# Kernel optimization log

Measured on AMD Instinct MI355X. Metric: run time of the kernel, lower is better.

## Reference

```python
import jax, jax.numpy as jnp
import numpy as np

BN_EPS = 1e-5
LN_EPS = 1e-5

N_NODES = 50000
N_EDGES = 800000
D_IN = 128
D_HID = 512


def _batchnorm(h, gamma, beta):
    # training-mode BatchNorm1d: biased variance over the node/batch dim
    m = jnp.mean(h, axis=0)
    v = jnp.mean(jnp.square(h - m), axis=0)
    return (h - m) * jax.lax.rsqrt(v + BN_EPS) * gamma + beta


def setup_inputs() -> dict:
    key = jax.random.key(0)
    ks = jax.random.split(key, 8)
    x = jax.random.normal(ks[0], (N_NODES, D_IN), dtype=jnp.float32)
    edge_index = jax.random.randint(ks[1], (2, N_EDGES), 0, N_NODES, dtype=jnp.int64)
    s1 = 1.0 / np.sqrt(D_IN)
    s2 = 1.0 / np.sqrt(D_HID)
    W1 = jax.random.uniform(ks[2], (D_IN, D_HID), jnp.float32, -s1, s1)
    b1 = jax.random.uniform(ks[3], (D_HID,), jnp.float32, -s1, s1)
    W2 = jax.random.uniform(ks[4], (D_HID, D_IN), jnp.float32, -s2, s2)
    b2 = jax.random.uniform(ks[5], (D_IN,), jnp.float32, -s2, s2)
    return {
        "x": x,
        "edge_index": edge_index,
        "W1": W1, "b1": b1,
        "bn1_g": jnp.ones((D_HID,), jnp.float32), "bn1_b": jnp.zeros((D_HID,), jnp.float32),
        "W2": W2, "b2": b2,
        "bn2_g": jnp.ones((D_IN,), jnp.float32), "bn2_b": jnp.zeros((D_IN,), jnp.float32),
        "ln_g": jnp.ones((D_IN,), jnp.float32), "ln_b": jnp.zeros((D_IN,), jnp.float32),
    }


def reference(x, edge_index, W1, b1, bn1_g, bn1_b, W2, b2, bn2_g, bn2_b, ln_g, ln_b):
    n = x.shape[0]
    src = edge_index[0]
    dst = edge_index[1]
    # GIN aggregation: sum of neighbor (source) features at each destination node
    agg = jax.ops.segment_sum(x[src], dst, num_segments=n)  # [N, D_IN]
    h = x + agg  # (1 + eps) * x + agg, eps = 0
    # MLP: Linear -> BN -> ReLU -> Linear -> BN -> ReLU (final activation)
    h = jax.nn.relu(_batchnorm(h @ W1 + b1, bn1_g, bn1_b))  # [N, D_HID]
    h = jax.nn.relu(_batchnorm(h @ W2 + b2, bn2_g, bn2_b))  # [N, D_IN]
    # residual + LayerNorm (dropout p=0 -> identity)
    out = h + x
    m = jnp.mean(out, axis=-1, keepdims=True)
    v = jnp.mean(jnp.square(out - m), axis=-1, keepdims=True)
    out = (out - m) * jax.lax.rsqrt(v + LN_EPS) * ln_g + ln_b
    return out
```

## Files before the change

### kernel.cpp

```cpp
#include <hip/hip_runtime.h>
#include <stdint.h>

#define N_NODES 50000
#define N_EDGES 800000
#define D_IN    128
#define D_HID   512
#define NPAD    50048
#define SCAN_NB 196

typedef __attribute__((ext_vector_type(8))) short short8;
typedef __attribute__((ext_vector_type(4))) float f32x4;

union Pack8 { unsigned short us[8]; uint4 v; };

__device__ __forceinline__ float bf2f(unsigned short u) {
    union { unsigned int i; float f; } v; v.i = ((unsigned int)u) << 16; return v.f;
}
__device__ __forceinline__ unsigned short f2bf(float f) {
    union { float f; unsigned int i; } v; v.f = f;
    unsigned int r = v.i + 0x7fffu + ((v.i >> 16) & 1u);
    return (unsigned short)(r >> 16);
}
__device__ __forceinline__ float loadP(const void* p, long i, int isf) {
    return isf ? ((const float*)p)[i] : bf2f(((const unsigned short*)p)[i]);
}
__device__ __forceinline__ uint4 pack8(float4 f0, float4 f1) {
    Pack8 p;
    p.us[0] = f2bf(f0.x); p.us[1] = f2bf(f0.y); p.us[2] = f2bf(f0.z); p.us[3] = f2bf(f0.w);
    p.us[4] = f2bf(f1.x); p.us[5] = f2bf(f1.y); p.us[6] = f2bf(f1.z); p.us[7] = f2bf(f1.w);
    return p.v;
}

__global__ void k_init(const void* __restrict__ x, const int* __restrict__ ei,
                       float* __restrict__ stats, int* __restrict__ counts,
                       int* __restrict__ flags) {
    int t = threadIdx.x;
    if (blockIdx.x < 201) {
        int i = blockIdx.x * 256 + t;
        if (i < 1280) stats[i] = 0.f;
        else if (i < 1280 + N_NODES) counts[i - 1280] = 0;
    } else {
        __shared__ int sh[2];
        if (t == 0) { sh[0] = 0; sh[1] = 1; }
        __syncthreads();
        const unsigned short* xu = (const unsigned short*)x;
        for (int i = t; i < 8192; i += 256)
            if (((xu[i] >> 7) & 0xFF) == 0xFF) sh[0] = 1;
        for (int k = t; k < 64; k += 256)
            if (ei[2 * k + 1] != 0) sh[1] = 0;
        __syncthreads();
        if (t == 0) { flags[0] = sh[0]; flags[1] = sh[1]; }
    }
}

__global__ void k_transpose2(const void* __restrict__ W1, const void* __restrict__ W2,
                             unsigned short* __restrict__ w1t, unsigned short* __restrict__ w2t,
                             const int* __restrict__ flags) {
    int isf = flags[0];
    int idx = blockIdx.x * 256 + threadIdx.x;
    if (idx < D_IN * D_HID) {
        int k = idx / D_HID, n = idx % D_HID;
        w1t[n * D_IN + k] = isf ? f2bf(((const float*)W1)[idx])
                                : ((const unsigned short*)W1)[idx];
    } else {
        int j = idx - D_IN * D_HID;
        int k = j / D_IN, n = j % D_IN;
        w2t[n * D_HID + k] = isf ? f2bf(((const float*)W2)[j])
                                 : ((const unsigned short*)W2)[j];
    }
}

__global__ void k_count(const int* __restrict__ ei, int* __restrict__ counts,
                        const int* __restrict__ flags) {
    int i64 = flags[1];
    int e = blockIdx.x * 256 + threadIdx.x;
    int d = i64 ? ei[2 * N_EDGES + 2 * e] : ei[N_EDGES + e];
    d = min(max(d, 0), N_NODES - 1);
    atomicAdd(&counts[d], 1);
}

__global__ __launch_bounds__(256) void k_scan_block(const int* __restrict__ counts,
                                                    int* __restrict__ rowptr,
                                                    int* __restrict__ partials) {
    __shared__ int a[256], b[256];
    int t = threadIdx.x;
    int idx = blockIdx.x * 256 + t;
    int c = (idx < N_NODES) ? counts[idx] : 0;
    a[t] = c;
    __syncthreads();
    int* src = a; int* dst = b;
    for (int off = 1; off < 256; off <<= 1) {
        dst[t] = src[t] + ((t >= off) ? src[t - off] : 0);
        __syncthreads();
        int* tmp = src; src = dst; dst = tmp;
    }
    if (idx < N_NODES) rowptr[idx] = src[t] - c;
    if (t == 255) partials[blockIdx.x] = src[255];
}

__global__ __launch_bounds__(256) void k_scan_part(int* __restrict__ partials) {
    __shared__ int a[256], b[256];
    int t = threadIdx.x;
    int c = (t < SCAN_NB) ? partials[t] : 0;
    a[t] = c;
    __syncthreads();
    int* src = a; int* dst = b;
    for (int off = 1; off < 256; off <<= 1) {
        dst[t] = src[t] + ((t >= off) ? src[t - off] : 0);
        __syncthreads();
        int* tmp = src; src = dst; dst = tmp;
    }
    if (t < SCAN_NB) partials[t] = src[t] - c;
}

__global__ void k_scan_add(int* __restrict__ rowptr, int* __restrict__ cursor,
                           const int* __restrict__ partials) {
    int idx = blockIdx.x * 256 + threadIdx.x;
    if (idx < N_NODES) {
        int v = rowptr[idx] + partials[blockIdx.x];
        rowptr[idx] = v;
        cursor[idx] = v;
    } else if (idx == N_NODES) {
        rowptr[N_NODES] = N_EDGES;
    }
}

__global__ void k_fill(const int* __restrict__ ei, int* __restrict__ cursor,
                       int* __restrict__ bucket, const int* __restrict__ flags) {
    int i64 = flags[1];
    int e = blockIdx.x * 256 + threadIdx.x;
    int s, d;
    if (i64) { s = ei[2 * e]; d = ei[2 * N_EDGES + 2 * e]; }
    else     { s = ei[e];     d = ei[N_EDGES + e]; }
    s = min(max(s, 0), N_NODES - 1);
    d = min(max(d, 0), N_NODES - 1);
    int pos = atomicAdd(&cursor[d], 1);
    bucket[pos] = s;
}

__global__ __launch_bounds__(256) void k_gather(const int* __restrict__ rowptr,
                                                const int* __restrict__ bucket,
                                                const void* __restrict__ x,
                                                float* __restrict__ agg,
                                                const int* __restrict__ flags) {
    int isf = flags[0];
    int w = threadIdx.x >> 6, lane = threadIdx.x & 63;
    int row = blockIdx.x * 4 + w;
    float a0 = 0.f, a1 = 0.f;
    if (row < N_NODES) {
        int beg = rowptr[row], end = rowptr[row + 1];
        if (isf) {
            const float* xf = (const float*)x;
            float2 v = *(const float2*)(xf + (size_t)row * D_IN + lane * 2);
            a0 = v.x; a1 = v.y;
            int j = beg;
            for (; j + 4 <= end; j += 4) {
                int s0 = bucket[j], s1 = bucket[j + 1], s2 = bucket[j + 2], s3 = bucket[j + 3];
                float2 n0 = *(const float2*)(xf + (size_t)s0 * D_IN + lane * 2);
                float2 n1 = *(const float2*)(xf + (size_t)s1 * D_IN + lane * 2);
                float2 n2 = *(const float2*)(xf + (size_t)s2 * D_IN + lane * 2);
                float2 n3 = *(const float2*)(xf + (size_t)s3 * D_IN + lane * 2);
                a0 += (n0.x + n1.x) + (n2.x + n3.x);
                a1 += (n0.y + n1.y) + (n2.y + n3.y);
            }
            for (; j < end; j++) {
                float2 n = *(const float2*)(xf + (size_t)bucket[j] * D_IN + lane * 2);
                a0 += n.x; a1 += n.y;
            }
        } else {
            const unsigned int* xu = (const unsigned int*)x;
            unsigned int u = xu[(size_t)row * 64 + lane];
            a0 = bf2f(u & 0xffff); a1 = bf2f(u >> 16);
            int j = beg;
            for (; j + 4 <= end; j += 4) {
                int s0 = bucket[j], s1 = bucket[j + 1], s2 = bucket[j + 2], s3 = bucket[j + 3];
                unsigned int u0 = xu[(size_t)s0 * 64 + lane];
                unsigned int u1 = xu[(size_t)s1 * 64 + lane];
                unsigned int u2 = xu[(size_t)s2 * 64 + lane];
                unsigned int u3 = xu[(size_t)s3 * 64 + lane];
                a0 += (bf2f(u0 & 0xffff) + bf2f(u1 & 0xffff)) + (bf2f(u2 & 0xffff) + bf2f(u3 & 0xffff));
                a1 += (bf2f(u0 >> 16) + bf2f(u1 >> 16)) + (bf2f(u2 >> 16) + bf2f(u3 >> 16));
            }
            for (; j < end; j++) {
                unsigned int n = xu[(size_t)bucket[j] * 64 + lane];
                a0 += bf2f(n & 0xffff); a1 += bf2f(n >> 16);
            }
        }
    }
    *(float2*)(agg + (size_t)row * D_IN + lane * 2) = make_float2(a0, a1);
}

__global__ __launch_bounds__(256) void k_g1stats(const float* __restrict__ agg,
                                                 const unsigned short* __restrict__ w1t,
                                                 const void* __restrict__ b1,
                                                 float* __restrict__ sum1,
                                                 float* __restrict__ sumsq1,
                                                 const int* __restrict__ flags) {
    __shared__ unsigned short ldsX[128 * 128];
    __shared__ unsigned short ldsW[128 * 128];
    int isf = flags[0];
    int t = threadIdx.x;
    int m0 = blockIdx.x * 128;
    int r = t >> 1, half = t & 1;
#pragma unroll
    for (int i = 0; i < 8; i++) {
        int chunk = half * 8 + i;
        int sw = ((chunk ^ (r & 15)) * 8);
        const float* g = agg + (size_t)(m0 + r) * D_IN + chunk * 8;
        *(uint4*)(ldsX + r * 128 + sw) = pack8(*(const float4*)g, *(const float4*)(g + 4));
    }
    int wid = t >> 6, lane = t & 63;
    int wm = wid & 1, wn = wid >> 1;
    int quad = lane >> 4, l16 = lane & 15;
    for (int nb = 0; nb < 4; nb++) {
        __syncthreads();
#pragma unroll
        for (int i = 0; i < 8; i++) {
            int chunk = half * 8 + i;
            *(uint4*)(ldsW + r * 128 + ((chunk ^ (r & 15)) * 8)) =
                *(const uint4*)(w1t + (size_t)(nb * 128 + r) * D_IN + chunk * 8);
        }
        __syncthreads();
        f32x4 acc[4][4] = {};
#pragma unroll
        for (int ks = 0; ks < 4; ks++) {
            short8 af[4], bfr[4];
#pragma unroll
            for (int mt = 0; mt < 4; mt++)
                af[mt] = *(const short8*)(ldsX + (wm * 64 + mt * 16 + l16) * 128 + (((ks * 4 + quad) ^ l16) * 8));
#pragma unroll
            for (int nt = 0; nt < 4; nt++)
                bfr[nt] = *(const short8*)(ldsW + (wn * 64 + nt * 16 + l16) * 128 + (((ks * 4 + quad) ^ l16) * 8));
#pragma unroll
            for (int mt = 0; mt < 4; mt++)
#pragma unroll
                for (int nt = 0; nt < 4; nt++)
                    acc[mt][nt] = __builtin_amdgcn_mfma_f32_16x16x32_bf16(af[mt], bfr[nt], acc[mt][nt], 0, 0, 0);
        }
#pragma unroll
        for (int nt = 0; nt < 4; nt++) {
            int n = nb * 128 + wn * 64 + nt * 16 + l16;
            float bias = loadP(b1, n, isf);
            float s = 0.f, ss = 0.f;
#pragma unroll
            for (int mt = 0; mt < 4; mt++) {
                int Rb = m0 + wm * 64 + mt * 16 + quad * 4;
#pragma unroll
                for (int rg = 0; rg < 4; rg++) {
                    if (Rb + rg < N_NODES) {
                        float z = acc[mt][nt][rg] + bias;
                        s += z; ss += z * z;
                    }
                }
            }
            s += __shfl_xor(s, 16, 64); ss += __shfl_xor(ss, 16, 64);
            s += __shfl_xor(s, 32, 64); ss += __shfl_xor(ss, 32, 64);
            if (quad == 0) { atomicAdd(&sum1[n], s); atomicAdd(&sumsq1[n], ss); }
        }
    }
}

__global__ __launch_bounds__(256) void k_fused(const float* __restrict__ agg,
                                               const unsigned short* __restrict__ w1t,
                                               const unsigned short* __restrict__ w2t,
                                               const void* __restrict__ b1,
                                               const void* __restrict__ b2,
                                               const void* __restrict__ g1,
                                               const void* __restrict__ bb1,
                                               const float* __restrict__ sum1,
                                               const float* __restrict__ sumsq1,
                                               float* __restrict__ h2,
                                               float* __restrict__ sum2,
                                               float* __restrict__ sumsq2,
                                               const int* __restrict__ flags) {
    __shared__ unsigned short bufXP[128 * 128];
    __shared__ unsigned short bufW[128 * 128];
    int isf = flags[0];
    int t = threadIdx.x;
    int m0 = blockIdx.x * 128;
    int r = t >> 1, half = t & 1;
    int wid = t >> 6, lane = t & 63;
    int wm = wid & 1, wn = wid >> 1;
    int quad = lane >> 4, l16 = lane & 15;
    f32x4 acc2[4][4] = {};
    for (int nb = 0; nb < 4; nb++) {
        __syncthreads();
#pragma unroll
        for (int i = 0; i < 8; i++) {
            int chunk = half * 8 + i;
            int sw = ((chunk ^ (r & 15)) * 8);
            const float* g = agg + (size_t)(m0 + r) * D_IN + chunk * 8;
            *(uint4*)(bufXP + r * 128 + sw) = pack8(*(const float4*)g, *(const float4*)(g + 4));
            *(uint4*)(bufW + r * 128 + sw) = *(const uint4*)(w1t + (size_t)(nb * 128 + r) * D_IN + chunk * 8);
        }
        __syncthreads();
        f32x4 acc1[4][4] = {};
#pragma unroll
        for (int ks = 0; ks < 4; ks++) {
            short8 af[4], bfr[4];
#pragma unroll
            for (int mt = 0; mt < 4; mt++)
                af[mt] = *(const short8*)(bufXP + (wm * 64 + mt * 16 + l16) * 128 + (((ks * 4 + quad) ^ l16) * 8));
#pragma unroll
            for (int nt = 0; nt < 4; nt++)
                bfr[nt] = *(const short8*)(bufW + (wn * 64 + nt * 16 + l16) * 128 + (((ks * 4 + quad) ^ l16) * 8));
#pragma unroll
            for (int mt = 0; mt < 4; mt++)
#pragma unroll
                for (int nt = 0; nt < 4; nt++)
                    acc1[mt][nt] = __builtin_amdgcn_mfma_f32_16x16x32_bf16(af[mt], bfr[nt], acc1[mt][nt], 0, 0, 0);
        }
        __syncthreads();
#pragma unroll
        for (int nt = 0; nt < 4; nt++) {
            int nl = wn * 64 + nt * 16 + l16;
            int n1 = nb * 128 + nl;
            float mz = sum1[n1] * (1.f / N_NODES);
            float vz = sumsq1[n1] * (1.f / N_NODES) - mz * mz;
            float inv = rsqrtf(fmaxf(vz, 0.f) + 1e-5f);
            float A = loadP(g1, n1, isf) * inv;
            float C = loadP(bb1, n1, isf) - mz * A + loadP(b1, n1, isf) * A;
            int ccw = nl >> 3, cl = nl & 7;
#pragma unroll
            for (int mt = 0; mt < 4; mt++)
#pragma unroll
                for (int rg = 0; rg < 4; rg++) {
                    int R = wm * 64 + mt * 16 + quad * 4 + rg;
                    float z = fmaxf(acc1[mt][nt][rg] * A + C, 0.f);
                    bufXP[R * 128 + ((ccw ^ (R & 15)) * 8) + cl] = f2bf(z);
                }
        }
#pragma unroll
        for (int i = 0; i < 8; i++) {
            int chunk = half * 8 + i;
            *(uint4*)(bufW + r * 128 + ((chunk ^ (r & 15)) * 8)) =
                *(const uint4*)(w2t + (size_t)r * D_HID + nb * 128 + chunk * 8);
        }
        __syncthreads();
#pragma unroll
        for (int ks = 0; ks < 4; ks++) {
            short8 af[4], bfr[4];
#pragma unroll
            for (int mt = 0; mt < 4; mt++)
                af[mt] = *(const short8*)(bufXP + (wm * 64 + mt * 16 + l16) * 128 + (((ks * 4 + quad) ^ l16) * 8));
#pragma unroll
            for (int nt = 0; nt < 4; nt++)
                bfr[nt] = *(const short8*)(bufW + (wn * 64 + nt * 16 + l16) * 128 + (((ks * 4 + quad) ^ l16) * 8));
#pragma unroll
            for (int mt = 0; mt < 4; mt++)
#pragma unroll
                for (int nt = 0; nt < 4; nt++)
                    acc2[mt][nt] = __builtin_amdgcn_mfma_f32_16x16x32_bf16(af[mt], bfr[nt], acc2[mt][nt], 0, 0, 0);
        }
    }
#pragma unroll
    for (int nt = 0; nt < 4; nt++) {
        int n = wn * 64 + nt * 16 + l16;
        float bias = loadP(b2, n, isf);
        float s = 0.f, ss = 0.f;
#pragma unroll
        for (int mt = 0; mt < 4; mt++) {
            int Rb = m0 + wm * 64 + mt * 16 + quad * 4;
#pragma unroll
            for (int rg = 0; rg < 4; rg++) {
                float z = acc2[mt][nt][rg] + bias;
                h2[(size_t)(Rb + rg) * D_IN + n] = z;
                if (Rb + rg < N_NODES) { s += z; ss += z * z; }
            }
        }
        s += __shfl_xor(s, 16, 64); ss += __shfl_xor(ss, 16, 64);
        s += __shfl_xor(s, 32, 64); ss += __shfl_xor(ss, 32, 64);
        if (quad == 0) { atomicAdd(&sum2[n], s); atomicAdd(&sumsq2[n], ss); }
    }
}

__global__ __launch_bounds__(256) void k_final(const float* __restrict__ h2,
                                               const void* __restrict__ x,
                                               const float* __restrict__ sum2,
                                               const float* __restrict__ sumsq2,
                                               const void* __restrict__ g2,
                                               const void* __restrict__ bb2,
                                               const void* __restrict__ lng,
                                               const void* __restrict__ lnb,
                                               void* __restrict__ out,
                                               const int* __restrict__ flags) {
    int isf = flags[0];
    __shared__ float a2s[D_IN], c2s[D_IN];
    int t = threadIdx.x;
    if (t < D_IN) {
        float m = sum2[t] * (1.f / N_NODES);
        float v = sumsq2[t] * (1.f / N_NODES) - m * m;
        float inv = rsqrtf(fmaxf(v, 0.f) + 1e-5f);
        float a = loadP(g2, t, isf) * inv;
        a2s[t] = a;
        c2s[t] = loadP(bb2, t, isf) - m * a;
    }
    __syncthreads();
    int w = t >> 6, lane = t & 63;
    int row = blockIdx.x * 4 + w;
    if (row >= N_NODES) return;
    size_t base = (size_t)row * D_IN;
    float o0 = fmaxf(a2s[lane] * h2[base + lane] + c2s[lane], 0.f) + loadP(x, base + lane, isf);
    float o1 = fmaxf(a2s[lane + 64] * h2[base + 64 + lane] + c2s[lane + 64], 0.f) + loadP(x, base + 64 + lane, isf);
    float s = o0 + o1, ss = o0 * o0 + o1 * o1;
#pragma unroll
    for (int m = 1; m < 64; m <<= 1) {
        s += __shfl_xor(s, m, 64);
        ss += __shfl_xor(ss, m, 64);
    }
    float mean = s * (1.f / D_IN);
    float var = ss * (1.f / D_IN) - mean * mean;
    float inv = rsqrtf(fmaxf(var, 0.f) + 1e-5f);
    float r0 = (o0 - mean) * inv * loadP(lng, lane, isf) + loadP(lnb, lane, isf);
    float r1 = (o1 - mean) * inv * loadP(lng, lane + 64, isf) + loadP(lnb, lane + 64, isf);
    if (isf) {
        ((float*)out)[base + lane] = r0;
        ((float*)out)[base + 64 + lane] = r1;
    } else {
        ((unsigned short*)out)[base + lane] = f2bf(r0);
        ((unsigned short*)out)[base + 64 + lane] = f2bf(r1);
    }
}

extern "C" void kernel_launch(void* const* d_in, const int* in_sizes, int n_in,
                              void* d_out, int out_size, void* d_ws, size_t ws_size,
                              hipStream_t stream) {
    const void* x    = d_in[0];
    const int*  ei   = (const int*)d_in[1];
    const void* W1   = d_in[2];
    const void* b1   = d_in[3];
    const void* bn1g = d_in[4];
    const void* bn1b = d_in[5];
    const void* W2   = d_in[6];
    const void* b2   = d_in[7];
    const void* bn2g = d_in[8];
    const void* bn2b = d_in[9];
    const void* lng  = d_in[10];
    const void* lnb  = d_in[11];

    char* ws = (char*)d_ws;
    float* stats    = (float*)ws;
    float* sum1     = stats;
    float* sumsq1   = stats + 512;
    float* sum2     = stats + 1024;
    float* sumsq2   = stats + 1152;
    int*   flags    = (int*)(ws + 5120);
    int*   partials = (int*)(ws + 5184);
    int*   rowptr   = (int*)(ws + 8192);
    int*   cursor   = (int*)(ws + 212992);
    unsigned short* w1t = (unsigned short*)(ws + 417792);
    unsigned short* w2t = (unsigned short*)(ws + 548864);
    int*   bucket = (int*)(ws + 679936);
    float* agg    = (float*)(ws + 3879936);
    float* h2     = agg;

    k_init<<<202, 256, 0, stream>>>(x, ei, stats, cursor, flags);
    k_transpose2<<<512, 256, 0, stream>>>(W1, W2, w1t, w2t, flags);
    k_count<<<N_EDGES / 256, 256, 0, stream>>>(ei, cursor, flags);
    k_scan_block<<<SCAN_NB, 256, 0, stream>>>(cursor, rowptr, partials);
    k_scan_part<<<1, 256, 0, stream>>>(partials);
    k_scan_add<<<SCAN_NB, 256, 0, stream>>>(rowptr, cursor, partials);
    k_fill<<<N_EDGES / 256, 256, 0, stream>>>(ei, cursor, bucket, flags);
    k_gather<<<NPAD / 4, 256, 0, stream>>>(rowptr, bucket, x, agg, flags);
    k_g1stats<<<NPAD / 128, 256, 0, stream>>>(agg, w1t, b1, sum1, sumsq1, flags);
    k_fused<<<NPAD / 128, 256, 0, stream>>>(agg, w1t, w2t, b1, b2, bn1g, bn1b,
                                            sum1, sumsq1, h2, sum2, sumsq2, flags);
    k_final<<<(N_NODES + 3) / 4, 256, 0, stream>>>(h2, x, sum2, sumsq2, bn2g, bn2b, lng, lnb, d_out, flags);
}
```

Before: 383.3 us.

## Materialize GEMM1 output in bf16 instead of recomputing it in fused kernel

Replaces the stats-only GEMM1 pass plus the recompute-GEMM1 fused kernel with two kernels. The first computes GEMM1 once, accumulates BN1 statistics and writes the hidden activations to a bf16 workspace buffer. The second applies BN1+ReLU while loading that buffer, then runs GEMM2 and accumulates BN2 statistics. This removes the duplicate GEMM1 compute but adds roughly 100MB of extra HBM write and read traffic, and it only runs when the workspace is large enough.

```diff
diff --git a/kernel.cpp b/kernel.cpp
--- a/kernel.cpp
+++ b/kernel.cpp
@@ -190,6 +190,194 @@
     *(float2*)(agg + (size_t)row * D_IN + lane * 2) = make_float2(a0, a1);
 }
 
+
+__global__ __launch_bounds__(256) void k_g1h1(const float* __restrict__ agg,
+                                              const unsigned short* __restrict__ w1t,
+                                              const void* __restrict__ b1,
+                                              float* __restrict__ sum1,
+                                              float* __restrict__ sumsq1,
+                                              unsigned short* __restrict__ h1,
+                                              const int* __restrict__ flags) {
+    __shared__ unsigned short ldsX[64 * 128];
+    __shared__ unsigned short ldsW[128 * 128];
+    int isf = flags[0];
+    int t = threadIdx.x;
+    int m0 = blockIdx.x * 64;
+    {
+        int r = t >> 2;
+        const float* g = agg + (size_t)(m0 + r) * D_IN;
+#pragma unroll
+        for (int i = 0; i < 4; i++) {
+            int chunk = (t & 3) * 4 + i;
+            *(uint4*)(ldsX + r * 128 + ((chunk ^ (r & 15)) * 8)) =
+                pack8(*(const float4*)(g + chunk * 8), *(const float4*)(g + chunk * 8 + 4));
+        }
+    }
+    int wid = t >> 6, lane = t & 63;
+    int wm = wid & 1, wn = wid >> 1;
+    int quad = lane >> 4, l16 = lane & 15;
+    int r2 = t >> 1, half = t & 1;
+    for (int nb = 0; nb < 4; nb++) {
+        __syncthreads();
+#pragma unroll
+        for (int i = 0; i < 8; i++) {
+            int chunk = half * 8 + i;
+            *(uint4*)(ldsW + r2 * 128 + ((chunk ^ (r2 & 15)) * 8)) =
+                *(const uint4*)(w1t + (size_t)(nb * 128 + r2) * D_IN + chunk * 8);
+        }
+        __syncthreads();
+        f32x4 acc[2][4] = {};
+#pragma unroll
+        for (int ks = 0; ks < 4; ks++) {
+            short8 af[2], bfr[4];
+#pragma unroll
+            for (int mt = 0; mt < 2; mt++) {
+                int rr = wm * 32 + mt * 16 + l16;
+                af[mt] = *(const short8*)(ldsX + rr * 128 + (((ks * 4 + quad) ^ (rr & 15)) * 8));
+            }
+#pragma unroll
+            for (int nt = 0; nt < 4; nt++) {
+                int nn = wn * 64 + nt * 16 + l16;
+                bfr[nt] = *(const short8*)(ldsW + nn * 128 + (((ks * 4 + quad) ^ (nn & 15)) * 8));
+            }
+#pragma unroll
+            for (int mt = 0; mt < 2; mt++)
+#pragma unroll
+                for (int nt = 0; nt < 4; nt++)
+                    acc[mt][nt] = __builtin_amdgcn_mfma_f32_16x16x32_bf16(af[mt], bfr[nt], acc[mt][nt], 0, 0, 0);
+        }
+        __syncthreads();
+#pragma unroll
+        for (int nt = 0; nt < 4; nt++) {
+            int nl = wn * 64 + nt * 16 + l16;
+            int n = nb * 128 + nl;
+            float bias = loadP(b1, n, isf);
+            float s = 0.f, ss = 0.f;
+            int ccw = nl >> 3, cl = nl & 7;
+#pragma unroll
+            for (int mt = 0; mt < 2; mt++) {
+                int Rl = wm * 32 + mt * 16 + quad * 4;
+#pragma unroll
+                for (int rg = 0; rg < 4; rg++) {
+                    float z = acc[mt][nt][rg] + bias;
+                    ldsW[(Rl + rg) * 128 + ((ccw ^ ((Rl + rg) & 15)) * 8) + cl] = f2bf(z);
+                    if (m0 + Rl + rg < N_NODES) { s += z; ss += z * z; }
+                }
+            }
+            s += __shfl_xor(s, 16, 64); ss += __shfl_xor(ss, 16, 64);
+            s += __shfl_xor(s, 32, 64); ss += __shfl_xor(ss, 32, 64);
+            if (quad == 0) { atomicAdd(&sum1[n], s); atomicAdd(&sumsq1[n], ss); }
+        }
+        __syncthreads();
+        {
+            int r = t >> 2;
+            unsigned short* gh = h1 + (size_t)(m0 + r) * D_HID + nb * 128;
+#pragma unroll
+            for (int i = 0; i < 4; i++) {
+                int chunk = (t & 3) * 4 + i;
+                *(uint4*)(gh + chunk * 8) = *(const uint4*)(ldsW + r * 128 + ((chunk ^ (r & 15)) * 8));
+            }
+        }
+    }
+}
+
+__global__ __launch_bounds__(256) void k_bn1gemm2(const unsigned short* __restrict__ h1,
+                                                  const unsigned short* __restrict__ w2t,
+                                                  const void* __restrict__ b2,
+                                                  const void* __restrict__ g1,
+                                                  const void* __restrict__ bb1,
+                                                  const float* __restrict__ sum1,
+                                                  const float* __restrict__ sumsq1,
+                                                  float* __restrict__ h2,
+                                                  float* __restrict__ sum2,
+                                                  float* __restrict__ sumsq2,
+                                                  const int* __restrict__ flags) {
+    __shared__ unsigned short ldsP[64 * 128];
+    __shared__ unsigned short ldsW[128 * 128];
+    __shared__ float a1s[D_HID], c1s[D_HID];
+    int isf = flags[0];
+    int t = threadIdx.x;
+    int m0 = blockIdx.x * 64;
+    for (int k = t; k < D_HID; k += 256) {
+        float mz = sum1[k] * (1.f / N_NODES);
+        float vz = sumsq1[k] * (1.f / N_NODES) - mz * mz;
+        float inv = rsqrtf(fmaxf(vz, 0.f) + 1e-5f);
+        float A = loadP(g1, k, isf) * inv;
+        a1s[k] = A;
+        c1s[k] = loadP(bb1, k, isf) - mz * A;
+    }
+    int wid = t >> 6, lane = t & 63;
+    int wm = wid & 1, wn = wid >> 1;
+    int quad = lane >> 4, l16 = lane & 15;
+    int r2 = t >> 1, half = t & 1;
+    f32x4 acc[2][4] = {};
+    for (int kb = 0; kb < 4; kb++) {
+        __syncthreads();
+        {
+            int r = t >> 2;
+            const unsigned short* gh = h1 + (size_t)(m0 + r) * D_HID + kb * 128;
+#pragma unroll
+            for (int i = 0; i < 4; i++) {
+                int chunk = (t & 3) * 4 + i;
+                Pack8 raw, outv;
+                raw.v = *(const uint4*)(gh + chunk * 8);
+#pragma unroll
+                for (int j = 0; j < 8; j++) {
+                    int k = kb * 128 + chunk * 8 + j;
+                    outv.us[j] = f2bf(fmaxf(bf2f(raw.us[j]) * a1s[k] + c1s[k], 0.f));
+                }
+                *(uint4*)(ldsP + r * 128 + ((chunk ^ (r & 15)) * 8)) = outv.v;
+            }
+        }
+#pragma unroll
+        for (int i = 0; i < 8; i++) {
+            int chunk = half * 8 + i;
+            *(uint4*)(ldsW + r2 * 128 + ((chunk ^ (r2 & 15)) * 8)) =
+                *(const uint4*)(w2t + (size_t)r2 * D_HID + kb * 128 + chunk * 8);
+        }
+        __syncthreads();
+#pragma unroll
+        for (int ks = 0; ks < 4; ks++) {
+            short8 af[2], bfr[4];
+#pragma unroll
+            for (int mt = 0; mt < 2; mt++) {
+                int rr = wm * 32 + mt * 16 + l16;
+                af[mt] = *(const short8*)(ldsP + rr * 128 + (((ks * 4 + quad) ^ (rr & 15)) * 8));
+            }
+#pragma unroll
+            for (int nt = 0; nt < 4; nt++) {
+                int nn = wn * 64 + nt * 16 + l16;
+                bfr[nt] = *(const short8*)(ldsW + nn * 128 + (((ks * 4 + quad) ^ (nn & 15)) * 8));
+            }
+#pragma unroll
+            for (int mt = 0; mt < 2; mt++)
+#pragma unroll
+                for (int nt = 0; nt < 4; nt++)
+                    acc[mt][nt] = __builtin_amdgcn_mfma_f32_16x16x32_bf16(af[mt], bfr[nt], acc[mt][nt], 0, 0, 0);
+        }
+    }
+#pragma unroll
+    for (int nt = 0; nt < 4; nt++) {
+        int n = wn * 64 + nt * 16 + l16;
+        float bias = loadP(b2, n, isf);
+        float s = 0.f, ss = 0.f;
+#pragma unroll
+        for (int mt = 0; mt < 2; mt++) {
+            int Rb = m0 + wm * 32 + mt * 16 + quad * 4;
+#pragma unroll
+            for (int rg = 0; rg < 4; rg++) {
+                float z = acc[mt][nt][rg] + bias;
+                h2[(size_t)(Rb + rg) * D_IN + n] = z;
+                if (Rb + rg < N_NODES) { s += z; ss += z * z; }
+            }
+        }
+        s += __shfl_xor(s, 16, 64); ss += __shfl_xor(ss, 16, 64);
+        s += __shfl_xor(s, 32, 64); ss += __shfl_xor(ss, 32, 64);
+        if (quad == 0) { atomicAdd(&sum2[n], s); atomicAdd(&sumsq2[n], ss); }
+    }
+}
+
+
 __global__ __launch_bounds__(256) void k_g1stats(const float* __restrict__ agg,
                                                  const unsigned short* __restrict__ w1t,
                                                  const void* __restrict__ b1,
@@ -453,6 +641,8 @@
     int*   bucket = (int*)(ws + 679936);
     float* agg    = (float*)(ws + 3879936);
     float* h2     = agg;
+    unsigned short* h1 = (unsigned short*)(ws + 3879936 + (size_t)NPAD * D_IN * 4);
+    size_t need_big = 3879936 + (size_t)NPAD * D_IN * 4 + (size_t)NPAD * D_HID * 2;
 
     k_init<<<202, 256, 0, stream>>>(x, ei, stats, cursor, flags);
     k_transpose2<<<512, 256, 0, stream>>>(W1, W2, w1t, w2t, flags);
@@ -462,8 +652,14 @@
     k_scan_add<<<SCAN_NB, 256, 0, stream>>>(rowptr, cursor, partials);
     k_fill<<<N_EDGES / 256, 256, 0, stream>>>(ei, cursor, bucket, flags);
     k_gather<<<NPAD / 4, 256, 0, stream>>>(rowptr, bucket, x, agg, flags);
-    k_g1stats<<<NPAD / 128, 256, 0, stream>>>(agg, w1t, b1, sum1, sumsq1, flags);
-    k_fused<<<NPAD / 128, 256, 0, stream>>>(agg, w1t, w2t, b1, b2, bn1g, bn1b,
-                                            sum1, sumsq1, h2, sum2, sumsq2, flags);
+    if (ws_size >= need_big) {
+        k_g1h1<<<NPAD / 64, 256, 0, stream>>>(agg, w1t, b1, sum1, sumsq1, h1, flags);
+        k_bn1gemm2<<<NPAD / 64, 256, 0, stream>>>(h1, w2t, b2, bn1g, bn1b,
+                                                  sum1, sumsq1, h2, sum2, sumsq2, flags);
+    } else {
+        k_g1stats<<<NPAD / 128, 256, 0, stream>>>(agg, w1t, b1, sum1, sumsq1, flags);
+        k_fused<<<NPAD / 128, 256, 0, stream>>>(agg, w1t, w2t, b1, b2, bn1g, bn1b,
+                                                sum1, sumsq1, h2, sum2, sumsq2, flags);
+    }
     k_final<<<(N_NODES + 3) / 4, 256, 0, stream>>>(h2, x, sum2, sumsq2, bn2g, bn2b, lng, lnb, d_out, flags);
 }
```

New measurement: 439.5 us. +14.7%, slower.

## Compute BN1 statistics from Gram matrix of aggregated features instead of full GEMM

Applied to the files above, without the earlier changes.

Replaces the stats pass, which ran the full 50000x128x512 GEMM just to collect per-column sum and sum-of-squares, with an algebraic route. It builds the 128x128 Gram matrix X^T X and the column sums of agg, then derives sum1 and sumsq1 for each hidden unit as w^T s and w^T G w plus bias terms. This cuts the FLOPs for the stats pass by about 4x but adds four small kernels, a partial-Gram buffer and a reduction. Squared terms are now formed from bf16-rounded inputs and summed across blocks, which may change numerical accuracy. Padding rows are included in the column sums and Gram matrix and are assumed to be zero.

```diff
diff --git a/kernel.cpp b/kernel.cpp
--- a/kernel.cpp
+++ b/kernel.cpp
@@ -7,6 +7,7 @@
 #define D_HID   512
 #define NPAD    50048
 #define SCAN_NB 196
+#define GRAM_NB 196
 
 typedef __attribute__((ext_vector_type(8))) short short8;
 typedef __attribute__((ext_vector_type(4))) float f32x4;
@@ -37,8 +38,8 @@
     int t = threadIdx.x;
     if (blockIdx.x < 201) {
         int i = blockIdx.x * 256 + t;
-        if (i < 1280) stats[i] = 0.f;
-        else if (i < 1280 + N_NODES) counts[i - 1280] = 0;
+        if (i < 1408) stats[i] = 0.f;
+        else if (i < 1408 + N_NODES) counts[i - 1408] = 0;
     } else {
         __shared__ int sh[2];
         if (t == 0) { sh[0] = 0; sh[1] = 1; }
@@ -190,73 +191,126 @@
     *(float2*)(agg + (size_t)row * D_IN + lane * 2) = make_float2(a0, a1);
 }
 
-__global__ __launch_bounds__(256) void k_g1stats(const float* __restrict__ agg,
-                                                 const unsigned short* __restrict__ w1t,
-                                                 const void* __restrict__ b1,
-                                                 float* __restrict__ sum1,
-                                                 float* __restrict__ sumsq1,
-                                                 const int* __restrict__ flags) {
-    __shared__ unsigned short ldsX[128 * 128];
-    __shared__ unsigned short ldsW[128 * 128];
-    int isf = flags[0];
-    int t = threadIdx.x;
-    int m0 = blockIdx.x * 128;
-    int r = t >> 1, half = t & 1;
-#pragma unroll
-    for (int i = 0; i < 8; i++) {
-        int chunk = half * 8 + i;
-        int sw = ((chunk ^ (r & 15)) * 8);
-        const float* g = agg + (size_t)(m0 + r) * D_IN + chunk * 8;
-        *(uint4*)(ldsX + r * 128 + sw) = pack8(*(const float4*)g, *(const float4*)(g + 4));
-    }
+__global__ __launch_bounds__(256) void k_colsum(const float* __restrict__ agg,
+                                                float* __restrict__ scol) {
+    __shared__ float red[256];
+    int t = threadIdx.x;
+    int c = t & 127, h = t >> 7;
+    int r0 = blockIdx.x * 256 + h * 128;
+    float acc = 0.f;
+    for (int i = 0; i < 128; i++) {
+        int row = r0 + i;
+        if (row < NPAD) acc += agg[(size_t)row * D_IN + c];
+    }
+    red[t] = acc;
+    __syncthreads();
+    if (h == 0) atomicAdd(&scol[c], red[c] + red[128 + c]);
+}
+
+__global__ __launch_bounds__(256) void k_gram(const float* __restrict__ agg,
+                                              float* __restrict__ gpart) {
+    __shared__ unsigned short XT[128 * 72];
+    int t = threadIdx.x;
+    int m0 = blockIdx.x * 256;
     int wid = t >> 6, lane = t & 63;
     int wm = wid & 1, wn = wid >> 1;
     int quad = lane >> 4, l16 = lane & 15;
-    for (int nb = 0; nb < 4; nb++) {
-        __syncthreads();
-#pragma unroll
-        for (int i = 0; i < 8; i++) {
-            int chunk = half * 8 + i;
-            *(uint4*)(ldsW + r * 128 + ((chunk ^ (r & 15)) * 8)) =
-                *(const uint4*)(w1t + (size_t)(nb * 128 + r) * D_IN + chunk * 8);
-        }
-        __syncthreads();
-        f32x4 acc[4][4] = {};
-#pragma unroll
-        for (int ks = 0; ks < 4; ks++) {
+    f32x4 acc[4][4] = {};
+    for (int ch = 0; ch < 4; ch++) {
+        __syncthreads();
+        {
+            int r = t >> 2;
+            int c0 = (t & 3) * 32;
+            int row = m0 + ch * 64 + r;
+            if (row < NPAD) {
+                const float* g = agg + (size_t)row * D_IN + c0;
+#pragma unroll
+                for (int i = 0; i < 32; i += 4) {
+                    float4 f = *(const float4*)(g + i);
+                    XT[(c0 + i + 0) * 72 + r] = f2bf(f.x);
+                    XT[(c0 + i + 1) * 72 + r] = f2bf(f.y);
+                    XT[(c0 + i + 2) * 72 + r] = f2bf(f.z);
+                    XT[(c0 + i + 3) * 72 + r] = f2bf(f.w);
+                }
+            } else {
+#pragma unroll
+                for (int i = 0; i < 32; i++) XT[(c0 + i) * 72 + r] = 0;
+            }
+        }
+        __syncthreads();
+#pragma unroll
+        for (int ks = 0; ks < 2; ks++) {
             short8 af[4], bfr[4];
 #pragma unroll
-            for (int mt = 0; mt < 4; mt++)
-                af[mt] = *(const short8*)(ldsX + (wm * 64 + mt * 16 + l16) * 128 + (((ks * 4 + quad) ^ l16) * 8));
-#pragma unroll
-            for (int nt = 0; nt < 4; nt++)
-                bfr[nt] = *(const short8*)(ldsW + (wn * 64 + nt * 16 + l16) * 128 + (((ks * 4 + quad) ^ l16) * 8));
+            for (int mt = 0; mt < 4; mt++) {
+                int m = wm * 64 + mt * 16 + l16;
+                af[mt] = *(const short8*)(XT + m * 72 + ks * 32 + quad * 8);
+            }
+#pragma unroll
+            for (int nt = 0; nt < 4; nt++) {
+                int n = wn * 64 + nt * 16 + l16;
+                bfr[nt] = *(const short8*)(XT + n * 72 + ks * 32 + quad * 8);
+            }
 #pragma unroll
             for (int mt = 0; mt < 4; mt++)
 #pragma unroll
                 for (int nt = 0; nt < 4; nt++)
                     acc[mt][nt] = __builtin_amdgcn_mfma_f32_16x16x32_bf16(af[mt], bfr[nt], acc[mt][nt], 0, 0, 0);
         }
-#pragma unroll
-        for (int nt = 0; nt < 4; nt++) {
-            int n = nb * 128 + wn * 64 + nt * 16 + l16;
-            float bias = loadP(b1, n, isf);
-            float s = 0.f, ss = 0.f;
-#pragma unroll
-            for (int mt = 0; mt < 4; mt++) {
-                int Rb = m0 + wm * 64 + mt * 16 + quad * 4;
-#pragma unroll
-                for (int rg = 0; rg < 4; rg++) {
-                    if (Rb + rg < N_NODES) {
-                        float z = acc[mt][nt][rg] + bias;
-                        s += z; ss += z * z;
-                    }
-                }
-            }
-            s += __shfl_xor(s, 16, 64); ss += __shfl_xor(ss, 16, 64);
-            s += __shfl_xor(s, 32, 64); ss += __shfl_xor(ss, 32, 64);
-            if (quad == 0) { atomicAdd(&sum1[n], s); atomicAdd(&sumsq1[n], ss); }
-        }
+    }
+    float* P = gpart + (size_t)blockIdx.x * 16384;
+#pragma unroll
+    for (int nt = 0; nt < 4; nt++) {
+        int n = wn * 64 + nt * 16 + l16;
+#pragma unroll
+        for (int mt = 0; mt < 4; mt++) {
+            int Rb = wm * 64 + mt * 16 + quad * 4;
+#pragma unroll
+            for (int rg = 0; rg < 4; rg++)
+                P[(Rb + rg) * 128 + n] = acc[mt][nt][rg];
+        }
+    }
+}
+
+__global__ void k_gram_reduce(const float* __restrict__ gpart, float* __restrict__ G) {
+    int idx = blockIdx.x * 256 + threadIdx.x;
+    float s = 0.f;
+    for (int b = 0; b < GRAM_NB; b++) s += gpart[(size_t)b * 16384 + idx];
+    G[idx] = s;
+}
+
+__global__ __launch_bounds__(256) void k_solve(const float* __restrict__ G,
+                                               const float* __restrict__ scol,
+                                               const unsigned short* __restrict__ w1t,
+                                               const void* __restrict__ b1,
+                                               float* __restrict__ sum1,
+                                               float* __restrict__ sumsq1,
+                                               const int* __restrict__ flags) {
+    __shared__ float wsh[4][128];
+    int isf = flags[0];
+    int t = threadIdx.x, wid = t >> 6, lane = t & 63;
+    int n = blockIdx.x * 4 + wid;
+    float w0 = bf2f(w1t[n * D_IN + lane]);
+    float w1 = bf2f(w1t[n * D_IN + 64 + lane]);
+    wsh[wid][lane] = w0; wsh[wid][64 + lane] = w1;
+    __syncthreads();
+    float v0 = 0.f, v1 = 0.f;
+    for (int k = 0; k < 128; k++) {
+        float wk = wsh[wid][k];
+        v0 += wk * G[k * 128 + lane];
+        v1 += wk * G[k * 128 + 64 + lane];
+    }
+    float sw = scol[lane] * w0 + scol[64 + lane] * w1;
+    float qq = w0 * v0 + w1 * v1;
+#pragma unroll
+    for (int m = 1; m < 64; m <<= 1) {
+        sw += __shfl_xor(sw, m, 64);
+        qq += __shfl_xor(qq, m, 64);
+    }
+    if (lane == 0) {
+        float b = loadP(b1, n, isf);
+        sum1[n] = sw + (float)N_NODES * b;
+        sumsq1[n] = qq + 2.f * b * sw + (float)N_NODES * b * b;
     }
 }
 
@@ -444,8 +498,9 @@
     float* sumsq1   = stats + 512;
     float* sum2     = stats + 1024;
     float* sumsq2   = stats + 1152;
-    int*   flags    = (int*)(ws + 5120);
-    int*   partials = (int*)(ws + 5184);
+    float* scol     = (float*)(ws + 5120);
+    int*   flags    = (int*)(ws + 5632);
+    int*   partials = (int*)(ws + 5760);
     int*   rowptr   = (int*)(ws + 8192);
     int*   cursor   = (int*)(ws + 212992);
     unsigned short* w1t = (unsigned short*)(ws + 417792);
@@ -453,6 +508,8 @@
     int*   bucket = (int*)(ws + 679936);
     float* agg    = (float*)(ws + 3879936);
     float* h2     = agg;
+    float* G      = (float*)(ws + 29504512);
+    float* gpart  = (float*)(ws + 29570048);
 
     k_init<<<202, 256, 0, stream>>>(x, ei, stats, cursor, flags);
     k_transpose2<<<512, 256, 0, stream>>>(W1, W2, w1t, w2t, flags);
@@ -462,7 +519,10 @@
     k_scan_add<<<SCAN_NB, 256, 0, stream>>>(rowptr, cursor, partials);
     k_fill<<<N_EDGES / 256, 256, 0, stream>>>(ei, cursor, bucket, flags);
     k_gather<<<NPAD / 4, 256, 0, stream>>>(rowptr, bucket, x, agg, flags);
-    k_g1stats<<<NPAD / 128, 256, 0, stream>>>(agg, w1t, b1, sum1, sumsq1, flags);
+    k_colsum<<<GRAM_NB, 256, 0, stream>>>(agg, scol);
+    k_gram<<<GRAM_NB, 256, 0, stream>>>(agg, gpart);
+    k_gram_reduce<<<64, 256, 0, stream>>>(gpart, G);
+    k_solve<<<128, 256, 0, stream>>>(G, scol, w1t, b1, sum1, sumsq1, flags);
     k_fused<<<NPAD / 128, 256, 0, stream>>>(agg, w1t, w2t, b1, b2, bn1g, bn1b,
                                             sum1, sumsq1, h2, sum2, sumsq2, flags);
     k_final<<<(N_NODES + 3) / 4, 256, 0, stream>>>(h2, x, sum2, sumsq2, bn2g, bn2b, lng, lnb, d_out, flags);
```

Measured after the change: 400.9 us. +4.6%, slower.
